# Performance work log

Hardware: AMD Instinct MI355X
Metric: run time of the kernel (lower is better)

The kernel has to match this reference:

```python
import jax, jax.numpy as jnp
import numpy as np

D = 1024   # input_size / width
H = 1024   # hidden_size / lru_width
TW = 4     # conv1d temporal width (Griffin default)
C_GATE = 8.0


def setup_inputs() -> dict:
    key = jax.random.key(0)
    ks = jax.random.split(key, 12)
    B, T = 8, 4096
    sd = 1.0 / np.sqrt(D)
    sh = 1.0 / np.sqrt(H)
    return {
        "input_bxtxd": jax.random.normal(ks[0], (B, T, D), jnp.float32),
        "w_x": jax.random.normal(ks[1], (D, H), jnp.float32) * sd,
        "b_x": jnp.zeros((H,), jnp.float32),
        "w_y": jax.random.normal(ks[2], (D, H), jnp.float32) * sd,
        "b_y": jnp.zeros((H,), jnp.float32),
        "conv_w": jax.random.normal(ks[3], (TW, H), jnp.float32) * 0.5,
        "conv_b": jnp.zeros((H,), jnp.float32),
        "gi_w": jax.random.normal(ks[4], (H, H), jnp.float32) * sh,
        "gi_b": jnp.zeros((H,), jnp.float32),
        "ga_w": jax.random.normal(ks[5], (H, H), jnp.float32) * sh,
        "ga_b": jnp.zeros((H,), jnp.float32),
        # a_param > 0 so a = exp(-c*gate*softplus(a_param)) lies in (0,1)
        "a_param": jax.random.uniform(ks[6], (H,), jnp.float32, 2.0, 6.0),
    }


def reference(input_bxtxd, w_x, b_x, w_y, b_y, conv_w, conv_b,
              gi_w, gi_b, ga_w, ga_b, a_param):
    x = input_bxtxd                      # [B,T,D], batch_first
    B, T, _ = x.shape

    # x branch: linear_x -> causal depthwise conv1d (zero cache) -> RG-LRU
    x1 = jnp.einsum("btd,dh->bth", x, w_x) + b_x            # [B,T,H]
    xp = jnp.pad(x1, ((0, 0), (TW - 1, 0), (0, 0)))          # causal pad
    x2 = sum(conv_w[i] * xp[:, i:i + T, :] for i in range(TW)) + conv_b

    # RG-LRU gates (num_heads=1 -> full linear)
    gate_x = jax.nn.sigmoid(jnp.einsum("bth,hk->btk", x2, gi_w) + gi_b)
    gate_a = jax.nn.sigmoid(jnp.einsum("bth,hk->btk", x2, ga_w) + ga_b)
    log_a = -C_GATE * gate_a * jax.nn.softplus(a_param)      # [B,T,H]
    a = jnp.exp(log_a)
    multiplier = jnp.sqrt(jnp.maximum(1.0 - jnp.exp(2.0 * log_a), 0.0))
    # segment_pos = arange(T): reset at t == 0
    multiplier = multiplier.at[:, 0, :].set(1.0)
    a = a.at[:, 0, :].set(0.0)
    normalized_x = gate_x * x2 * multiplier                  # [B,T,H]

    # linear recurrence h_t = a_t * h_{t-1} + normalized_x_t (h_{-1}=0)
    def combine(c1, c2):
        a1, h1 = c1
        a2, h2 = c2
        return a1 * a2, h2 + a2 * h1

    _, h = jax.lax.associative_scan(combine, (a, normalized_x), axis=1)

    # y branch and output gating
    y = jax.nn.gelu(jnp.einsum("btd,dh->bth", x, w_y) + b_y, approximate=False)
    out = h * y                                              # [B,T,H]
    hn = h[:, -1, :]                                         # last state
    return out, h, hn
```

## Files before the change

kernel.cpp:

```cpp
#include <hip/hip_runtime.h>
#include <math.h>


#define B_ 8
#define T_ 4096
#define H_ 1024
#define M_ (B_ * T_)
#define NC_ 128
#define CL_ 32

typedef _Float16 half8 __attribute__((ext_vector_type(8)));
typedef _Float16 half4 __attribute__((ext_vector_type(4)));
typedef float    f32x4 __attribute__((ext_vector_type(4)));

__device__ __forceinline__ void load16_lds(const _Float16* g, _Float16* l) {
  __builtin_amdgcn_global_load_lds(
      (const __attribute__((address_space(1))) void*)g,
      (__attribute__((address_space(3))) void*)l, 16, 0, 0);
}

__global__ __launch_bounds__(256) void transpose_cvt(
    const float* __restrict__ sA, const float* __restrict__ sB,
    _Float16* __restrict__ dst) {
  __shared__ float tile[32][33];
  int bn = blockIdx.x * 32;
  int bk = blockIdx.y * 32;
  const float* src = (bn < 1024) ? sA : sB;
  int nof = (bn < 1024) ? bn : bn - 1024;
  int c  = threadIdx.x & 31;
  int r0 = threadIdx.x >> 5;
#pragma unroll
  for (int i = 0; i < 4; ++i) {
    int r = r0 + i * 8;
    tile[r][c] = src[(size_t)(bk + r) * 1024 + nof + c];
  }
  __syncthreads();
#pragma unroll
  for (int i = 0; i < 4; ++i) {
    int nl = r0 + i * 8;
    dst[(size_t)(bn + nl) * 1024 + bk + c] = (_Float16)tile[c][nl];
  }
}

__global__ void prep_bias(const float* __restrict__ bx, const float* __restrict__ by,
                          const float* __restrict__ gib, const float* __restrict__ gab,
                          float* __restrict__ b1, float* __restrict__ b2) {
  int i = blockIdx.x * 1024 + threadIdx.x;
  if (i < 1024)      b1[i] = bx[i];
  else if (i < 2048) b1[i] = by[i - 1024];
  else if (i < 3072) b2[i - 2048] = gib[i - 2048];
  else               b2[i - 2048] = gab[i - 3072];
}

__global__ __launch_bounds__(256) void cvt_fp16(
    const float* __restrict__ x, _Float16* __restrict__ xh, long n4) {
  for (long i = (long)blockIdx.x * 256 + threadIdx.x; i < n4;
       i += (long)gridDim.x * 256) {
    f32x4 v = ((const f32x4*)x)[i];
    half4 h;
#pragma unroll
    for (int e = 0; e < 4; ++e) h[e] = (_Float16)v[e];
    ((half4*)xh)[i] = h;
  }
}

template <int MODE>
__global__ __launch_bounds__(256, 2) void gemm_kernel(
    const _Float16* __restrict__ A, const _Float16* __restrict__ Bt,
    const float* __restrict__ bias, const float* __restrict__ a_param,
    _Float16* __restrict__ C) {
  __shared__ _Float16 sA[128 * 32];
  __shared__ _Float16 sB[128 * 32];
  const int K = 1024;
  int tid  = threadIdx.x;
  int lane = tid & 63;
  int wave = tid >> 6;

  int nb  = (int)blockIdx.x;
  int per = (int)gridDim.x >> 3;
  nb = (nb & 7) * per + (nb >> 3);
  int mtile = nb >> 4;
  int ntile = nb & 15;
  int m0 = mtile * 128, n0 = ntile * 128;
  int wm = wave >> 1, wn = wave & 1;

  int row0 = tid >> 2, kg0 = tid & 3;
  const _Float16* gA0 = A  + (size_t)(m0 + row0) * K + kg0 * 8;
  const _Float16* gA1 = gA0 + (size_t)64 * K;
  const _Float16* gB0 = Bt + (size_t)(n0 + row0) * K + kg0 * 8;
  const _Float16* gB1 = gB0 + (size_t)64 * K;
  _Float16* lA0 = sA + wave * 512;
  _Float16* lA1 = sA + 2048 + wave * 512;
  _Float16* lB0 = sB + wave * 512;
  _Float16* lB1 = sB + 2048 + wave * 512;

  f32x4 acc[4][4];
  f32x4 zero = {0.f, 0.f, 0.f, 0.f};
#pragma unroll
  for (int i = 0; i < 4; ++i)
#pragma unroll
    for (int j = 0; j < 4; ++j) acc[i][j] = zero;

  const half8* sA8 = (const half8*)sA;
  const half8* sB8 = (const half8*)sB;
  int fa = (wm * 64 + (lane & 15)) * 4 + (lane >> 4);
  int fb = (wn * 64 + (lane & 15)) * 4 + (lane >> 4);

  for (int kk = 0; kk < 32; ++kk) {
    int ko = kk * 32;
    load16_lds(gA0 + ko, lA0);
    load16_lds(gA1 + ko, lA1);
    load16_lds(gB0 + ko, lB0);
    load16_lds(gB1 + ko, lB1);
    __syncthreads();
    half8 af[4], bf[4];
#pragma unroll
    for (int mi = 0; mi < 4; ++mi) af[mi] = sA8[fa + mi * 64];
#pragma unroll
    for (int ni = 0; ni < 4; ++ni) bf[ni] = sB8[fb + ni * 64];
#pragma unroll
    for (int mi = 0; mi < 4; ++mi)
#pragma unroll
      for (int ni = 0; ni < 4; ++ni)
        acc[mi][ni] = __builtin_amdgcn_mfma_f32_16x16x32_f16(
            af[mi], bf[ni], acc[mi][ni], 0, 0, 0);
    __syncthreads();
  }

  int lr = lane >> 4;
  int lc = lane & 15;
  int   gn[4];
  float bs[4], sp[4];
#pragma unroll
  for (int ni = 0; ni < 4; ++ni) {
    gn[ni] = n0 + wn * 64 + ni * 16 + lc;
    bs[ni] = bias[gn[ni]];
    sp[ni] = 0.f;
    if (MODE == 1 && gn[ni] >= 1024)
      sp[ni] = log1pf(expf(a_param[gn[ni] - 1024]));
  }
#pragma unroll
  for (int mi = 0; mi < 4; ++mi) {
#pragma unroll
    for (int p = 0; p < 4; ++p) {
      int gm = m0 + wm * 64 + mi * 16 + lr * 4 + p;
      size_t rowb = (size_t)gm * 2048;
#pragma unroll
      for (int ni = 0; ni < 4; ++ni) {
        float v = acc[mi][ni][p] + bs[ni];
        if (MODE == 1) {
          float s = 1.f / (1.f + expf(-v));
          if (gn[ni] < 1024) {
            v = s;
          } else {
            float a = expf(-8.f * s * sp[ni]);
            if ((gm & (T_ - 1)) == 0) a = 0.f;
            v = a;
          }
        }
        C[rowb + gn[ni]] = (_Float16)v;
      }
    }
  }
}

__global__ __launch_bounds__(256) void conv_kernel(
    const _Float16* __restrict__ g1, const float* __restrict__ cw,
    const float* __restrict__ cb, _Float16* __restrict__ x2) {
  int idx = blockIdx.x * 256 + threadIdx.x;
  int m  = idx >> 7;
  int hb = (idx & 127) * 8;
  int t  = m & (T_ - 1);
  float acc[8];
#pragma unroll
  for (int e = 0; e < 8; ++e) acc[e] = cb[hb + e];
#pragma unroll
  for (int j = 0; j < 4; ++j) {
    if (t >= j) {
      half8 xv = *(const half8*)&g1[(size_t)(m - j) * 2048 + hb];
      const float* w = &cw[(3 - j) * 1024 + hb];
#pragma unroll
      for (int e = 0; e < 8; ++e) acc[e] += w[e] * (float)xv[e];
    }
  }
  half8 o;
#pragma unroll
  for (int e = 0; e < 8; ++e) o[e] = (_Float16)acc[e];
  *(half8*)&x2[(size_t)m * 1024 + hb] = o;
}

__global__ __launch_bounds__(128) void scan1_kernel(
    const _Float16* __restrict__ g2, const _Float16* __restrict__ x2,
    float* __restrict__ cA, float* __restrict__ cH) {
  int bid = blockIdx.x;
  int b = bid >> 7, c = bid & 127;
  int h0 = threadIdx.x * 8;
  float A[8], Hh[8];
#pragma unroll
  for (int e = 0; e < 8; ++e) { A[e] = 1.f; Hh[e] = 0.f; }
  size_t mbase = (size_t)b * T_ + (size_t)c * CL_;
  for (int i = 0; i < CL_; ++i) {
    size_t m = mbase + i;
    half8 gx = *(const half8*)&g2[m * 2048 + h0];
    half8 av = *(const half8*)&g2[m * 2048 + 1024 + h0];
    half8 xv = *(const half8*)&x2[m * 1024 + h0];
#pragma unroll
    for (int e = 0; e < 8; ++e) {
      float a = (float)av[e];
      float mult = sqrtf(fmaxf(1.f - a * a, 0.f));
      float nx = (float)gx[e] * (float)xv[e] * mult;
      A[e] *= a;
      Hh[e] = nx + a * Hh[e];
    }
  }
  size_t o = (size_t)bid * 1024 + h0;
#pragma unroll
  for (int e = 0; e < 8; ++e) { cA[o + e] = A[e]; cH[o + e] = Hh[e]; }
}

__global__ void scanmid_kernel(const float* __restrict__ cA,
                               const float* __restrict__ cH,
                               float* __restrict__ carry) {
  int gidx = blockIdx.x * 256 + threadIdx.x;
  int b = gidx >> 10, h = gidx & 1023;
  float run = 0.f;
  for (int c = 0; c < NC_; ++c) {
    size_t o = ((size_t)(b * NC_ + c)) * 1024 + h;
    carry[o] = run;
    run = cH[o] + cA[o] * run;
  }
}

__global__ __launch_bounds__(128) void scan2_kernel(
    const _Float16* __restrict__ g2, const _Float16* __restrict__ x2,
    const _Float16* __restrict__ g1, const float* __restrict__ carry,
    float* __restrict__ outO, float* __restrict__ outH,
    float* __restrict__ outHn) {
  int bid = blockIdx.x;
  int b = bid >> 7, c = bid & 127;
  int h0 = threadIdx.x * 8;
  float Hh[8];
  {
    size_t o = (size_t)bid * 1024 + h0;
#pragma unroll
    for (int e = 0; e < 8; ++e) Hh[e] = carry[o + e];
  }
  size_t mbase = (size_t)b * T_ + (size_t)c * CL_;
  for (int i = 0; i < CL_; ++i) {
    size_t m = mbase + i;
    half8 gx = *(const half8*)&g2[m * 2048 + h0];
    half8 av = *(const half8*)&g2[m * 2048 + 1024 + h0];
    half8 xv = *(const half8*)&x2[m * 1024 + h0];
    half8 uv = *(const half8*)&g1[m * 2048 + 1024 + h0];
    f32x4 hO[2], oO[2];
#pragma unroll
    for (int e = 0; e < 8; ++e) {
      float a = (float)av[e];
      float mult = sqrtf(fmaxf(1.f - a * a, 0.f));
      float nx = (float)gx[e] * (float)xv[e] * mult;
      float v = nx + a * Hh[e];
      Hh[e] = v;
      float u = (float)uv[e];
      float y = 0.5f * u * (1.f + erff(u * 0.70710678118654752f));
      hO[e >> 2][e & 3] = v;
      oO[e >> 2][e & 3] = v * y;
    }
    size_t ob = m * 1024 + h0;
    *(f32x4*)&outH[ob]     = hO[0];
    *(f32x4*)&outH[ob + 4] = hO[1];
    *(f32x4*)&outO[ob]     = oO[0];
    *(f32x4*)&outO[ob + 4] = oO[1];
  }
  if (c == NC_ - 1) {
    size_t o = (size_t)b * 1024 + h0;
#pragma unroll
    for (int e = 0; e < 8; ++e) outHn[o + e] = Hh[e];
  }
}

extern "C" void kernel_launch(void* const* d_in, const int* in_sizes, int n_in,
                              void* d_out, int out_size, void* d_ws,
                              size_t ws_size, hipStream_t stream) {
  const float* x   = (const float*)d_in[0];
  const float* wx  = (const float*)d_in[1];
  const float* bx  = (const float*)d_in[2];
  const float* wy  = (const float*)d_in[3];
  const float* by  = (const float*)d_in[4];
  const float* cw  = (const float*)d_in[5];
  const float* cb  = (const float*)d_in[6];
  const float* giw = (const float*)d_in[7];
  const float* gib = (const float*)d_in[8];
  const float* gaw = (const float*)d_in[9];
  const float* gab = (const float*)d_in[10];
  const float* ap  = (const float*)d_in[11];

  char* ws = (char*)d_ws;
  size_t off = 0;
  auto alloc = [&](size_t bytes) {
    char* p = ws + off;
    off += (bytes + 255) & ~(size_t)255;
    return p;
  };
  _Float16* wT1 = (_Float16*)alloc((size_t)2048 * 1024 * 2);
  _Float16* wT2 = (_Float16*)alloc((size_t)2048 * 1024 * 2);
  float*    b1  = (float*)alloc(2048 * 4);
  float*    b2  = (float*)alloc(2048 * 4);
  _Float16* xh  = (_Float16*)alloc((size_t)M_ * 1024 * 2);
  _Float16* g2e = (_Float16*)alloc((size_t)M_ * 1024 * 2);
  (void)g2e;
  _Float16* g1o = (_Float16*)alloc((size_t)M_ * 2048 * 2);
  _Float16* x2h = (_Float16*)alloc((size_t)M_ * 1024 * 2);
  float* cA  = (float*)alloc((size_t)B_ * NC_ * 1024 * 4);
  float* cH  = (float*)alloc((size_t)B_ * NC_ * 1024 * 4);
  float* cin = (float*)alloc((size_t)B_ * NC_ * 1024 * 4);
  _Float16* g2o = xh;

  float* oO  = (float*)d_out;
  float* oH  = oO + (size_t)M_ * 1024;
  float* oHn = oO + (size_t)2 * M_ * 1024;

  transpose_cvt<<<dim3(64, 32), 256, 0, stream>>>(wx, wy, wT1);
  transpose_cvt<<<dim3(64, 32), 256, 0, stream>>>(giw, gaw, wT2);
  prep_bias<<<4, 1024, 0, stream>>>(bx, by, gib, gab, b1, b2);
  cvt_fp16<<<2048, 256, 0, stream>>>(x, xh, (long)M_ * 1024 / 4);

  gemm_kernel<0><<<4096, 256, 0, stream>>>(xh, wT1, b1, nullptr, g1o);
  conv_kernel<<<16384, 256, 0, stream>>>(g1o, cw, cb, x2h);
  gemm_kernel<1><<<4096, 256, 0, stream>>>(x2h, wT2, b2, ap, g2o);

  scan1_kernel<<<B_ * NC_, 128, 0, stream>>>(g2o, x2h, cA, cH);
  scanmid_kernel<<<32, 256, 0, stream>>>(cA, cH, cin);
  scan2_kernel<<<B_ * NC_, 128, 0, stream>>>(g2o, x2h, g1o, cin, oO, oH, oHn);
}
```

Measured before the change: 638.5 us.

## Rewrite GEMM with 256x256 tiles, double-buffered swizzled LDS and prefetch

Replaces the 128x128, 256-thread GEMM with a 256x256-tile, 512-thread kernel. It uses K-tiles of 64 with XOR-swizzled LDS to avoid bank conflicts, a double-buffered global-to-LDS prefetch of the next K-tile interleaved with the MFMA phases, and setprio around the MFMA blocks. The aim is more data reuse per block, overlap of memory loads with tensor-core work, and fewer redundant global reads. In exchange it uses 128 KB of LDS and 128 accumulator registers per thread, which limits occupancy and may cause register pressure or fail the 2-blocks-per-CU launch bound.

```diff
diff --git a/kernel.cpp b/kernel.cpp
--- a/kernel.cpp
+++ b/kernel.cpp
@@ -12,6 +12,10 @@
 typedef _Float16 half8 __attribute__((ext_vector_type(8)));
 typedef _Float16 half4 __attribute__((ext_vector_type(4)));
 typedef float    f32x4 __attribute__((ext_vector_type(4)));
+
+#define FENCE asm volatile("" ::: "memory")
+#define BAR() do { FENCE; __builtin_amdgcn_s_barrier(); FENCE; } while (0)
+#define MFMA16(a, b, c) __builtin_amdgcn_mfma_f32_16x16x32_f16((a), (b), (c), 0, 0, 0)
 
 __device__ __forceinline__ void load16_lds(const _Float16* g, _Float16* l) {
   __builtin_amdgcn_global_load_lds(
@@ -65,103 +69,156 @@
 }
 
 template <int MODE>
-__global__ __launch_bounds__(256, 2) void gemm_kernel(
+__global__ __launch_bounds__(512, 2) void gemm_kernel(
     const _Float16* __restrict__ A, const _Float16* __restrict__ Bt,
     const float* __restrict__ bias, const float* __restrict__ a_param,
     _Float16* __restrict__ C) {
-  __shared__ _Float16 sA[128 * 32];
-  __shared__ _Float16 sB[128 * 32];
-  const int K = 1024;
+  __shared__ _Float16 ldsA[32768];
+  __shared__ _Float16 ldsB[32768];
   int tid  = threadIdx.x;
   int lane = tid & 63;
   int wave = tid >> 6;
-
-  int nb  = (int)blockIdx.x;
-  int per = (int)gridDim.x >> 3;
-  nb = (nb & 7) * per + (nb >> 3);
-  int mtile = nb >> 4;
-  int ntile = nb & 15;
-  int m0 = mtile * 128, n0 = ntile * 128;
-  int wm = wave >> 1, wn = wave & 1;
-
-  int row0 = tid >> 2, kg0 = tid & 3;
-  const _Float16* gA0 = A  + (size_t)(m0 + row0) * K + kg0 * 8;
-  const _Float16* gA1 = gA0 + (size_t)64 * K;
-  const _Float16* gB0 = Bt + (size_t)(n0 + row0) * K + kg0 * 8;
-  const _Float16* gB1 = gB0 + (size_t)64 * K;
-  _Float16* lA0 = sA + wave * 512;
-  _Float16* lA1 = sA + 2048 + wave * 512;
-  _Float16* lB0 = sB + wave * 512;
-  _Float16* lB1 = sB + 2048 + wave * 512;
-
-  f32x4 acc[4][4];
-  f32x4 zero = {0.f, 0.f, 0.f, 0.f};
-#pragma unroll
-  for (int i = 0; i < 4; ++i)
-#pragma unroll
-    for (int j = 0; j < 4; ++j) acc[i][j] = zero;
-
-  const half8* sA8 = (const half8*)sA;
-  const half8* sB8 = (const half8*)sB;
-  int fa = (wm * 64 + (lane & 15)) * 4 + (lane >> 4);
-  int fb = (wn * 64 + (lane & 15)) * 4 + (lane >> 4);
-
-  for (int kk = 0; kk < 32; ++kk) {
-    int ko = kk * 32;
-    load16_lds(gA0 + ko, lA0);
-    load16_lds(gA1 + ko, lA1);
-    load16_lds(gB0 + ko, lB0);
-    load16_lds(gB1 + ko, lB1);
-    __syncthreads();
-    half8 af[4], bf[4];
-#pragma unroll
-    for (int mi = 0; mi < 4; ++mi) af[mi] = sA8[fa + mi * 64];
-#pragma unroll
-    for (int ni = 0; ni < 4; ++ni) bf[ni] = sB8[fb + ni * 64];
-#pragma unroll
-    for (int mi = 0; mi < 4; ++mi)
-#pragma unroll
-      for (int ni = 0; ni < 4; ++ni)
-        acc[mi][ni] = __builtin_amdgcn_mfma_f32_16x16x32_f16(
-            af[mi], bf[ni], acc[mi][ni], 0, 0, 0);
-    __syncthreads();
-  }
-
-  int lr = lane >> 4;
-  int lc = lane & 15;
+  int l15 = lane & 15, g = lane >> 4;
+
+  int nb = ((int)blockIdx.x & 7) * 128 + ((int)blockIdx.x >> 3);
+  int m0 = (nb >> 3) * 256;
+  int n0 = (nb & 7) * 256;
+  int wm = wave >> 2;
+  int wn = wave & 3;
+
+  int r0  = tid >> 3;
+  int blk = (tid & 7) ^ (r0 & 7);
+  const _Float16* pA = A  + (size_t)(m0 + r0) * 1024 + blk * 8;
+  const _Float16* pB = Bt + (size_t)(n0 + r0) * 1024 + blk * 8;
+  _Float16* stA = ldsA + wave * 512;
+  _Float16* stB = ldsB + wave * 512;
+
+#define STAGE_A(slot, mh, kt)                                                 \
+  do {                                                                        \
+    load16_lds(pA + (mh)*131072 + (kt)*64,         stA + (slot)*8192);        \
+    load16_lds(pA + (mh)*131072 + 65536 + (kt)*64, stA + (slot)*8192 + 4096); \
+  } while (0)
+#define STAGE_B(slot, nu, kt)                                                 \
+  do {                                                                        \
+    load16_lds(pB + (nu)*131072 + (kt)*64,         stB + (slot)*8192);        \
+    load16_lds(pB + (nu)*131072 + 65536 + (kt)*64, stB + (slot)*8192 + 4096); \
+  } while (0)
+
+  int xorf = (l15 & 7) << 3;
+  int xa0 = (g * 8) ^ xorf;
+  int xa1 = (32 + g * 8) ^ xorf;
+  int aBase = l15 * 64;
+  int bBase = ((wn & 1) * 64 + l15) * 64;
+  int bUnit = wn >> 1;
+
+  f32x4 acc[8][4];
+#pragma unroll
+  for (int i = 0; i < 8; ++i)
+#pragma unroll
+    for (int j = 0; j < 4; ++j) acc[i][j] = (f32x4){0.f, 0.f, 0.f, 0.f};
+
+  STAGE_A(0, 0, 0); STAGE_A(1, 1, 0);
+  STAGE_B(0, 0, 0); STAGE_B(1, 1, 0);
+  asm volatile("s_waitcnt vmcnt(0)" ::: "memory");
+  BAR();
+
+  half8 a[8], b0, b1;
+  for (int t = 0; t < 16; ++t) {
+    int db = (t & 1) << 1;
+    int dn = ((t + 1) & 1) << 1;
+    int aS = (db + wm) * 8192 + aBase;
+    int bS = (db + bUnit) * 8192 + bBase;
+    bool pre = (t < 15);
+
+#pragma unroll
+    for (int mi = 0; mi < 8; ++mi)
+      a[mi] = *(const half8*)(ldsA + aS + mi * 1024 + xa0);
+    b0 = *(const half8*)(ldsB + bS + xa0);
+    b1 = *(const half8*)(ldsB + bS + 1024 + xa0);
+    if (pre) { STAGE_A(dn, 0, t + 1); STAGE_B(dn, 0, t + 1); }
+    BAR();
+    __builtin_amdgcn_s_setprio(1);
+#pragma unroll
+    for (int mi = 0; mi < 8; ++mi) acc[mi][0] = MFMA16(a[mi], b0, acc[mi][0]);
+#pragma unroll
+    for (int mi = 0; mi < 8; ++mi) acc[mi][1] = MFMA16(a[mi], b1, acc[mi][1]);
+    __builtin_amdgcn_s_setprio(0);
+    BAR();
+
+    b0 = *(const half8*)(ldsB + bS + 2048 + xa0);
+    b1 = *(const half8*)(ldsB + bS + 3072 + xa0);
+    if (pre) { STAGE_A(dn + 1, 1, t + 1); STAGE_B(dn + 1, 1, t + 1); }
+    BAR();
+    __builtin_amdgcn_s_setprio(1);
+#pragma unroll
+    for (int mi = 0; mi < 8; ++mi) acc[mi][2] = MFMA16(a[mi], b0, acc[mi][2]);
+#pragma unroll
+    for (int mi = 0; mi < 8; ++mi) acc[mi][3] = MFMA16(a[mi], b1, acc[mi][3]);
+    __builtin_amdgcn_s_setprio(0);
+    BAR();
+
+#pragma unroll
+    for (int mi = 0; mi < 8; ++mi)
+      a[mi] = *(const half8*)(ldsA + aS + mi * 1024 + xa1);
+    b0 = *(const half8*)(ldsB + bS + xa1);
+    b1 = *(const half8*)(ldsB + bS + 1024 + xa1);
+    BAR();
+    __builtin_amdgcn_s_setprio(1);
+#pragma unroll
+    for (int mi = 0; mi < 8; ++mi) acc[mi][0] = MFMA16(a[mi], b0, acc[mi][0]);
+#pragma unroll
+    for (int mi = 0; mi < 8; ++mi) acc[mi][1] = MFMA16(a[mi], b1, acc[mi][1]);
+    __builtin_amdgcn_s_setprio(0);
+    BAR();
+
+    b0 = *(const half8*)(ldsB + bS + 2048 + xa1);
+    b1 = *(const half8*)(ldsB + bS + 3072 + xa1);
+    BAR();
+    __builtin_amdgcn_s_setprio(1);
+#pragma unroll
+    for (int mi = 0; mi < 8; ++mi) acc[mi][2] = MFMA16(a[mi], b0, acc[mi][2]);
+#pragma unroll
+    for (int mi = 0; mi < 8; ++mi) acc[mi][3] = MFMA16(a[mi], b1, acc[mi][3]);
+    __builtin_amdgcn_s_setprio(0);
+    asm volatile("s_waitcnt vmcnt(0)" ::: "memory");
+    BAR();
+  }
+
   int   gn[4];
   float bs[4], sp[4];
 #pragma unroll
-  for (int ni = 0; ni < 4; ++ni) {
-    gn[ni] = n0 + wn * 64 + ni * 16 + lc;
-    bs[ni] = bias[gn[ni]];
-    sp[ni] = 0.f;
-    if (MODE == 1 && gn[ni] >= 1024)
-      sp[ni] = log1pf(expf(a_param[gn[ni] - 1024]));
-  }
-#pragma unroll
-  for (int mi = 0; mi < 4; ++mi) {
+  for (int nj = 0; nj < 4; ++nj) {
+    gn[nj] = n0 + wn * 64 + nj * 16 + l15;
+    bs[nj] = bias[gn[nj]];
+    sp[nj] = 0.f;
+    if (MODE == 1 && gn[nj] >= 1024)
+      sp[nj] = log1pf(expf(a_param[gn[nj] - 1024]));
+  }
+#pragma unroll
+  for (int mi = 0; mi < 8; ++mi) {
 #pragma unroll
     for (int p = 0; p < 4; ++p) {
-      int gm = m0 + wm * 64 + mi * 16 + lr * 4 + p;
+      int gm = m0 + wm * 128 + mi * 16 + g * 4 + p;
       size_t rowb = (size_t)gm * 2048;
 #pragma unroll
-      for (int ni = 0; ni < 4; ++ni) {
-        float v = acc[mi][ni][p] + bs[ni];
+      for (int nj = 0; nj < 4; ++nj) {
+        float v = acc[mi][nj][p] + bs[nj];
         if (MODE == 1) {
           float s = 1.f / (1.f + expf(-v));
-          if (gn[ni] < 1024) {
+          if (gn[nj] < 1024) {
             v = s;
           } else {
-            float a = expf(-8.f * s * sp[ni]);
-            if ((gm & (T_ - 1)) == 0) a = 0.f;
-            v = a;
+            float av = expf(-8.f * s * sp[nj]);
+            if ((gm & (T_ - 1)) == 0) av = 0.f;
+            v = av;
           }
         }
-        C[rowb + gn[ni]] = (_Float16)v;
+        C[rowb + gn[nj]] = (_Float16)v;
       }
     }
   }
+#undef STAGE_A
+#undef STAGE_B
 }
 
 __global__ __launch_bounds__(256) void conv_kernel(
@@ -324,9 +381,9 @@
   prep_bias<<<4, 1024, 0, stream>>>(bx, by, gib, gab, b1, b2);
   cvt_fp16<<<2048, 256, 0, stream>>>(x, xh, (long)M_ * 1024 / 4);
 
-  gemm_kernel<0><<<4096, 256, 0, stream>>>(xh, wT1, b1, nullptr, g1o);
+  gemm_kernel<0><<<1024, 512, 0, stream>>>(xh, wT1, b1, nullptr, g1o);
   conv_kernel<<<16384, 256, 0, stream>>>(g1o, cw, cb, x2h);
-  gemm_kernel<1><<<4096, 256, 0, stream>>>(x2h, wT2, b2, ap, g2o);
+  gemm_kernel<1><<<1024, 512, 0, stream>>>(x2h, wT2, b2, ap, g2o);
 
   scan1_kernel<<<B_ * NC_, 128, 0, stream>>>(g2o, x2h, cA, cH);
   scanmid_kernel<<<32, 256, 0, stream>>>(cA, cH, cin);
```

After: 620.0 us. -2.9%, faster.
